# Kernel optimization log

Hardware: AMD Instinct MI355X
Metric: run time of the kernel (lower is better)

The kernel has to match this reference:

```python
import jax, jax.numpy as jnp
import numpy as np

ANG = 5  # angRes; n = ANG*ANG
EPS = 1e-12  # torch F.normalize eps

def _l2norm(x, axis):
    n = jnp.sqrt(jnp.sum(x * x, axis=axis, keepdims=True))
    return x / jnp.maximum(n, EPS)

def setup_inputs() -> dict:
    key = jax.random.key(0)
    kq, kk, kv = jax.random.split(key, 3)
    shape = (16, 16, 25, 16, 128)  # b c n h w
    return {
        "token_q": jax.random.normal(kq, shape, dtype=jnp.float32),
        "token_k": jax.random.normal(kk, shape, dtype=jnp.float32),
        "token_v": jax.random.normal(kv, shape, dtype=jnp.float32),
    }

def reference(token_q, token_k, token_v):
    b, c, n, h, w = token_q.shape
    u = v = ANG
    buffer = token_v

    def to_q(x):  # b c (u v) h w -> b (c h) (w u v)
        return x.reshape(b, c, u, v, h, w).transpose(0, 1, 4, 5, 2, 3).reshape(b, c * h, w * u * v)

    def to_k(x):  # b c (u v) h w -> b (w u v) (c h)
        return x.reshape(b, c, u, v, h, w).transpose(0, 5, 2, 3, 1, 4).reshape(b, w * u * v, c * h)

    unfold_q = _l2norm(to_q(token_q), axis=-1)      # [b, ch, wuv]
    unfold_k = _l2norm(to_k(token_k), axis=-2)      # [b, wuv, ch]
    unfold_v = to_q(token_v)                        # [b, ch, wuv]

    att = jnp.einsum('bts,bsr->btr', unfold_q, unfold_k)  # [b, ch, ch]
    size = c * h
    causal = jnp.tril(jnp.ones((size, size), dtype=bool))
    att = jnp.where(causal, att, jnp.float32(-1e15))
    att = jax.nn.softmax(att, axis=-1)

    out = jnp.einsum('btr,brs->bts', att, unfold_v)  # [b, ch, wuv]
    # b (c h) (w u v) -> b c (u v) h w
    out = out.reshape(b, c, h, w, u, v).transpose(0, 1, 4, 5, 2, 3).reshape(b, c, n, h, w)
    return out + buffer
```

## Files before the change

kernel.cpp:

```cpp
#include <hip/hip_runtime.h>
#include <math.h>

#define SB 819200
#define SC 51200
#define SN 2048
#define CH 256
#define NW 3200
#define NPARTS 10
#define PARTLEN 320
#define BK 32
#define NCH 10
#define SPART 1048576
#define G1BLOCKS 480

typedef __bf16 bf16x8 __attribute__((ext_vector_type(8)));
typedef __bf16 bf16x4 __attribute__((ext_vector_type(4)));
typedef __bf16 bf16x2 __attribute__((ext_vector_type(2)));
typedef float  f32x4  __attribute__((ext_vector_type(4)));

__device__ __forceinline__ bf16x8 cvt8(float4 a, float4 b) {
    bf16x8 r;
    r[0] = (__bf16)a.x; r[1] = (__bf16)a.y; r[2] = (__bf16)a.z; r[3] = (__bf16)a.w;
    r[4] = (__bf16)b.x; r[5] = (__bf16)b.y; r[6] = (__bf16)b.z; r[7] = (__bf16)b.w;
    return r;
}

__device__ __forceinline__ float dot4(float4 a) {
    return a.x * a.x + a.y * a.y + a.z * a.z + a.w * a.w;
}

__global__ __launch_bounds__(256, 2) void gemm1_kernel(const float* __restrict__ q,
                                                       const float* __restrict__ k,
                                                       float* __restrict__ Sp,
                                                       float* __restrict__ nq2p,
                                                       float* __restrict__ nk2p) {
    __shared__ alignas(16) float lds[16384];

    const int tid = threadIdx.x;
    const int lane = tid & 63;
    const int wave = tid >> 6;
    const int l15 = lane & 15;
    const int quad = lane >> 4;

    const int bx = blockIdx.x;
    const int tile = bx % 3;
    const int part = (bx / 3) % NPARTS;
    const int b = bx / (3 * NPARTS);
    const int tm = (tile + 1) >> 1;
    const int tn = tile >> 1;

    const int wm = wave >> 1;
    const int wn = wave & 1;

    const bool doQ = (tile != 2);
    const bool doK = (tile != 1);

    const int g8 = lane & 7;
    const int rl = lane >> 3;

    const float* qp[4];
    const float* kp[4];
#pragma unroll
    for (int i = 0; i < 4; i++) {
        const int row = wave * 32 + i * 8 + rl;
        const int ta = tm * 128 + row;
        const int rb = tn * 128 + row;
        qp[i] = q + (size_t)b * SB + (size_t)(ta >> 4) * SC + (size_t)(ta & 15) * 128 + g8 * 4;
        kp[i] = k + (size_t)b * SB + (size_t)(rb >> 4) * SC + (size_t)(rb & 15) * 128 + g8 * 4;
    }

    f32x4 acc[4][4] = {};
    bool live[4][4];
#pragma unroll
    for (int mi = 0; mi < 4; mi++)
#pragma unroll
        for (int ni = 0; ni < 4; ni++)
            live[mi][ni] = (tn * 128 + wn * 64 + ni * 16) <= (tm * 128 + wm * 64 + mi * 16);

    float sqA[4] = {0.f, 0.f, 0.f, 0.f};
    float sqB[4] = {0.f, 0.f, 0.f, 0.f};

    auto stage = [&](int ch, int p) {
        const int kg = part * PARTLEN + ch * BK;
        const size_t koff = (size_t)(kg >> 7) * SN + (kg & 127);
#pragma unroll
        for (int i = 0; i < 4; i++)
            __builtin_amdgcn_global_load_lds(
                (const __attribute__((address_space(1))) void*)(qp[i] + koff),
                (__attribute__((address_space(3))) void*)(&lds[p * 8192 + (wave * 4 + i) * 256]),
                16, 0, 0);
#pragma unroll
        for (int i = 0; i < 4; i++)
            __builtin_amdgcn_global_load_lds(
                (const __attribute__((address_space(1))) void*)(kp[i] + koff),
                (__attribute__((address_space(3))) void*)(&lds[p * 8192 + 4096 + (wave * 4 + i) * 256]),
                16, 0, 0);
    };

    stage(0, 0);

    for (int ch = 0; ch < NCH; ch++) {
        const int p = ch & 1;
        if (ch + 1 < NCH) {
            stage(ch + 1, 1 - p);
            asm volatile("s_waitcnt vmcnt(8)" ::: "memory");
        } else {
            asm volatile("s_waitcnt vmcnt(0)" ::: "memory");
        }
        __builtin_amdgcn_s_barrier();
        __builtin_amdgcn_sched_barrier(0);

        const float* A = &lds[p * 8192];
        const float* B = &lds[p * 8192 + 4096];
        bf16x8 af[4], bfr[4];
#pragma unroll
        for (int mi = 0; mi < 4; mi++) {
            const float4 lo = *(const float4*)&A[(wm * 64 + mi * 16 + l15) * 32 + quad * 8];
            const float4 hi = *(const float4*)&A[(wm * 64 + mi * 16 + l15) * 32 + quad * 8 + 4];
            af[mi] = cvt8(lo, hi);
            if (wn == 0) sqA[mi] += dot4(lo) + dot4(hi);
        }
#pragma unroll
        for (int ni = 0; ni < 4; ni++) {
            const float4 lo = *(const float4*)&B[(wn * 64 + ni * 16 + l15) * 32 + quad * 8];
            const float4 hi = *(const float4*)&B[(wn * 64 + ni * 16 + l15) * 32 + quad * 8 + 4];
            bfr[ni] = cvt8(lo, hi);
            if (wm == 0) sqB[ni] += dot4(lo) + dot4(hi);
        }
#pragma unroll
        for (int mi = 0; mi < 4; mi++)
#pragma unroll
            for (int ni = 0; ni < 4; ni++)
                if (live[mi][ni])
                    acc[mi][ni] = __builtin_amdgcn_mfma_f32_16x16x32_bf16(
                        af[mi], bfr[ni], acc[mi][ni], 0, 0, 0);

        __builtin_amdgcn_sched_barrier(0);
        __builtin_amdgcn_s_barrier();
        __builtin_amdgcn_sched_barrier(0);
    }

    float* o = Sp + (size_t)part * SPART + (size_t)b * 65536;
#pragma unroll
    for (int mi = 0; mi < 4; mi++)
#pragma unroll
        for (int ni = 0; ni < 4; ni++) {
            if (!live[mi][ni]) continue;
            const int r = tn * 128 + wn * 64 + ni * 16 + l15;
#pragma unroll
            for (int j = 0; j < 4; j++) {
                const int t = tm * 128 + wm * 64 + mi * 16 + quad * 4 + j;
                o[(size_t)t * 256 + r] = acc[mi][ni][j];
            }
        }

    if (wn == 0 && doQ) {
#pragma unroll
        for (int mi = 0; mi < 4; mi++) {
            float s = sqA[mi];
            s += __shfl_xor(s, 16, 64);
            s += __shfl_xor(s, 32, 64);
            if (lane < 16)
                nq2p[part * 4096 + b * 256 + tm * 128 + wm * 64 + mi * 16 + lane] = s;
        }
    }
    if (wm == 0 && doK) {
#pragma unroll
        for (int ni = 0; ni < 4; ni++) {
            float s = sqB[ni];
            s += __shfl_xor(s, 16, 64);
            s += __shfl_xor(s, 32, 64);
            if (lane < 16)
                nk2p[part * 4096 + b * 256 + tn * 128 + wn * 64 + ni * 16 + lane] = s;
        }
    }
}

__global__ __launch_bounds__(256) void softmax_kernel(const float* __restrict__ Sp,
                                                      const float* __restrict__ nq2p,
                                                      const float* __restrict__ nk2p,
                                                      __bf16* __restrict__ P) {
    const int wave = threadIdx.x >> 6;
    const int lane = threadIdx.x & 63;
    const int t = blockIdx.x * 4 + wave;
    const int b = blockIdx.y;
    const size_t rowbase = ((size_t)b * 256 + t) * 256;
    const int r0 = lane * 4;

    float4 s4 = {0.f, 0.f, 0.f, 0.f};
#pragma unroll
    for (int p = 0; p < NPARTS; p++) {
        const float4 x = *(const float4*)(Sp + (size_t)p * SPART + rowbase + r0);
        s4.x += x.x; s4.y += x.y; s4.z += x.z; s4.w += x.w;
    }
    float sq = 0.f;
#pragma unroll
    for (int p = 0; p < NPARTS; p++) sq += nq2p[p * 4096 + b * 256 + t];
    float4 sk = {0.f, 0.f, 0.f, 0.f};
#pragma unroll
    for (int p = 0; p < NPARTS; p++) {
        const float4 x = *(const float4*)(nk2p + p * 4096 + b * 256 + r0);
        sk.x += x.x; sk.y += x.y; sk.z += x.z; sk.w += x.w;
    }
    const float qn = 1.0f / fmaxf(sqrtf(sq), 1e-12f);
    float4 kn;
    kn.x = 1.0f / fmaxf(sqrtf(sk.x), 1e-12f);
    kn.y = 1.0f / fmaxf(sqrtf(sk.y), 1e-12f);
    kn.z = 1.0f / fmaxf(sqrtf(sk.z), 1e-12f);
    kn.w = 1.0f / fmaxf(sqrtf(sk.w), 1e-12f);

    float val[4] = {s4.x * qn * kn.x, s4.y * qn * kn.y,
                    s4.z * qn * kn.z, s4.w * qn * kn.w};
    float m = -1e30f;
#pragma unroll
    for (int j = 0; j < 4; j++) {
        if (r0 + j > t) val[j] = -1e30f;
        m = fmaxf(m, val[j]);
    }
#pragma unroll
    for (int off = 32; off; off >>= 1) m = fmaxf(m, __shfl_xor(m, off, 64));

    float e[4], sum = 0.f;
#pragma unroll
    for (int j = 0; j < 4; j++) {
        e[j] = (r0 + j <= t) ? expf(val[j] - m) : 0.f;
        sum += e[j];
    }
#pragma unroll
    for (int off = 32; off; off >>= 1) sum += __shfl_xor(sum, off, 64);

    const float inv = 1.0f / sum;
    bf16x4 o;
    o[0] = (__bf16)(e[0] * inv);
    o[1] = (__bf16)(e[1] * inv);
    o[2] = (__bf16)(e[2] * inv);
    o[3] = (__bf16)(e[3] * inv);
    *(bf16x4*)(P + rowbase + r0) = o;
}

__global__ __launch_bounds__(256, 4) void gemm2_kernel(const __bf16* __restrict__ P,
                                                       const float* __restrict__ v,
                                                       float* __restrict__ out) {
    __shared__ alignas(16) char smem[9216];
    __bf16* Vs = (__bf16*)smem;
    float* Es = (float*)smem;

    const int tid = threadIdx.x;
    const int b = blockIdx.z;
    const int tt = blockIdx.y;
    const int nw = blockIdx.x;
    const int n = nw >> 1;
    const int whalf = nw & 1;

    const int lane = tid & 63;
    const int wave = tid >> 6;
    const int wm = wave >> 1;
    const int wn = wave & 1;
    const int l15 = lane & 15;
    const int quad = lane >> 4;

    const int vu = tid & 7;
    const int rp = tid >> 3;
    const float* vbase = v + (size_t)b * SB + (size_t)n * SN + whalf * 64;

    const __bf16* Pbase = P + ((size_t)b * 256 + tt * 128 + wm * 64 + l15) * 256 + quad * 8;

    f32x4 acc[4][2] = {};

    for (int kc = 0; kc < 4; kc++) {
        bf16x8 af[4][2];
#pragma unroll
        for (int mi = 0; mi < 4; mi++)
#pragma unroll
            for (int ks = 0; ks < 2; ks++)
                af[mi][ks] = *(const bf16x8*)(Pbase + (size_t)mi * 16 * 256 + kc * 64 + ks * 32);

        float vr0[8], vr1[8];
        {
            const int r0 = kc * 64 + 2 * rp;
            const int r1 = r0 + 1;
            const float* row0 = vbase + (size_t)(r0 >> 4) * SC + (size_t)(r0 & 15) * 128;
            const float* row1 = vbase + (size_t)(r1 >> 4) * SC + (size_t)(r1 & 15) * 128;
            *(float4*)&vr0[0] = *(const float4*)(row0 + vu * 8);
            *(float4*)&vr0[4] = *(const float4*)(row0 + vu * 8 + 4);
            *(float4*)&vr1[0] = *(const float4*)(row1 + vu * 8);
            *(float4*)&vr1[4] = *(const float4*)(row1 + vu * 8 + 4);
        }
        __syncthreads();
        {
            const int rl0 = 2 * rp;
#pragma unroll
            for (int sj = 0; sj < 8; sj++) {
                const int s = vu * 8 + sj;
                bf16x2 pr;
                pr[0] = (__bf16)vr0[sj];
                pr[1] = (__bf16)vr1[sj];
                *(bf16x2*)&Vs[s * 72 + (rl0 ^ (s & 0x38))] = pr;
            }
        }
        __syncthreads();
#pragma unroll
        for (int ks = 0; ks < 2; ks++) {
            bf16x8 bfr[2];
#pragma unroll
            for (int ni = 0; ni < 2; ni++) {
                const int s = wn * 32 + ni * 16 + l15;
                bfr[ni] = *(const bf16x8*)&Vs[s * 72 + ((ks * 32 + quad * 8) ^ (s & 0x38))];
            }
#pragma unroll
            for (int mi = 0; mi < 4; mi++)
#pragma unroll
                for (int ni = 0; ni < 2; ni++)
                    acc[mi][ni] = __builtin_amdgcn_mfma_f32_16x16x32_bf16(
                        af[mi][ks], bfr[ni], acc[mi][ni], 0, 0, 0);
        }
    }

    for (int p = 0; p < 4; p++) {
        __syncthreads();
        if (wm == (p >> 1)) {
            const int mibase = (p & 1) * 2;
#pragma unroll
            for (int mm = 0; mm < 2; mm++)
#pragma unroll
                for (int ni = 0; ni < 2; ni++) {
                    const f32x4 a = acc[mibase + mm][ni];
                    const int wcol = wn * 32 + ni * 16 + l15;
#pragma unroll
                    for (int j = 0; j < 4; j++)
                        Es[(mm * 16 + quad * 4 + j) * 68 + wcol] = a[j];
                }
        }
        __syncthreads();
#pragma unroll
        for (int it = 0; it < 2; it++) {
            const int tl = it * 16 + (tid >> 4);
            const int w4 = (tid & 15) * 4;
            const int t = tt * 128 + p * 32 + tl;
            const size_t a = (size_t)b * SB + (size_t)(t >> 4) * SC + (size_t)n * SN +
                             (size_t)(t & 15) * 128 + whalf * 64 + w4;
            float4 r4 = *(const float4*)&Es[tl * 68 + w4];
            const float4 buf = *(const float4*)(v + a);
            r4.x += buf.x; r4.y += buf.y; r4.z += buf.z; r4.w += buf.w;
            *(float4*)(out + a) = r4;
        }
    }
}

extern "C" void kernel_launch(void* const* d_in, const int* in_sizes, int n_in,
                              void* d_out, int out_size, void* d_ws, size_t ws_size,
                              hipStream_t stream) {
    const float* q = (const float*)d_in[0];
    const float* k = (const float*)d_in[1];
    const float* v = (const float*)d_in[2];
    float* out = (float*)d_out;

    float* ws = (float*)d_ws;
    float* nq2p = ws;
    float* nk2p = ws + 40960;
    __bf16* P = (__bf16*)(ws + 81920);

    float* Spart = out;

    gemm1_kernel<<<dim3(G1BLOCKS), dim3(256), 0, stream>>>(q, k, Spart, nq2p, nk2p);
    softmax_kernel<<<dim3(64, 16), dim3(256), 0, stream>>>(Spart, nq2p, nk2p, P);
    gemm2_kernel<<<dim3(50, 2, 16), dim3(256), 0, stream>>>(P, v, out);
}
```

Before: 232.2 us.

## Load GEMM1 operands directly to registers with double buffering, dropping LDS staging

Replaces the LDS double-buffer staging (global_load_lds plus barriers) in gemm1 with direct per-wave global float4 loads into two register buffer sets, software-pipelined across 10 k-steps. This removes workgroup barriers and the LDS round trip. In exchange, data shared between waves is now loaded redundantly from global/L2, and register pressure rises, which may reduce occupancy under launch_bounds(256,2).

```diff
diff --git a/kernel.cpp b/kernel.cpp
--- a/kernel.cpp
+++ b/kernel.cpp
@@ -8,8 +8,7 @@
 #define NW 3200
 #define NPARTS 10
 #define PARTLEN 320
-#define BK 32
-#define NCH 10
+#define NSTEP 10
 #define SPART 1048576
 #define G1BLOCKS 480
 
@@ -34,8 +33,6 @@
                                                        float* __restrict__ Sp,
                                                        float* __restrict__ nq2p,
                                                        float* __restrict__ nk2p) {
-    __shared__ alignas(16) float lds[16384];
-
     const int tid = threadIdx.x;
     const int lane = tid & 63;
     const int wave = tid >> 6;
@@ -55,18 +52,14 @@
     const bool doQ = (tile != 2);
     const bool doK = (tile != 1);
 
-    const int g8 = lane & 7;
-    const int rl = lane >> 3;
-
-    const float* qp[4];
-    const float* kp[4];
+    const float* qrow[4];
+    const float* krow[4];
 #pragma unroll
     for (int i = 0; i < 4; i++) {
-        const int row = wave * 32 + i * 8 + rl;
-        const int ta = tm * 128 + row;
-        const int rb = tn * 128 + row;
-        qp[i] = q + (size_t)b * SB + (size_t)(ta >> 4) * SC + (size_t)(ta & 15) * 128 + g8 * 4;
-        kp[i] = k + (size_t)b * SB + (size_t)(rb >> 4) * SC + (size_t)(rb & 15) * 128 + g8 * 4;
+        const int ta = tm * 128 + wm * 64 + i * 16 + l15;
+        const int rb = tn * 128 + wn * 64 + i * 16 + l15;
+        qrow[i] = q + (size_t)b * SB + (size_t)(ta >> 4) * SC + (size_t)(ta & 15) * 128 + quad * 8;
+        krow[i] = k + (size_t)b * SB + (size_t)(rb >> 4) * SC + (size_t)(rb & 15) * 128 + quad * 8;
     }
 
     f32x4 acc[4][4] = {};
@@ -80,52 +73,36 @@
     float sqA[4] = {0.f, 0.f, 0.f, 0.f};
     float sqB[4] = {0.f, 0.f, 0.f, 0.f};
 
-    auto stage = [&](int ch, int p) {
-        const int kg = part * PARTLEN + ch * BK;
-        const size_t koff = (size_t)(kg >> 7) * SN + (kg & 127);
-#pragma unroll
-        for (int i = 0; i < 4; i++)
-            __builtin_amdgcn_global_load_lds(
-                (const __attribute__((address_space(1))) void*)(qp[i] + koff),
-                (__attribute__((address_space(3))) void*)(&lds[p * 8192 + (wave * 4 + i) * 256]),
-                16, 0, 0);
-#pragma unroll
-        for (int i = 0; i < 4; i++)
-            __builtin_amdgcn_global_load_lds(
-                (const __attribute__((address_space(1))) void*)(kp[i] + koff),
-                (__attribute__((address_space(3))) void*)(&lds[p * 8192 + 4096 + (wave * 4 + i) * 256]),
-                16, 0, 0);
+    float4 aL0[4], aH0[4], bL0[4], bH0[4];
+    float4 aL1[4], aH1[4], bL1[4], bH1[4];
+
+    auto loadstep = [&](int j, float4* aL, float4* aH, float4* bL, float4* bH) {
+        const int kgb = part * PARTLEN + j * 32;
+        const size_t koff = (size_t)(kgb >> 7) * SN + (kgb & 127);
+#pragma unroll
+        for (int i = 0; i < 4; i++) {
+            aL[i] = *(const float4*)(qrow[i] + koff);
+            aH[i] = *(const float4*)(qrow[i] + koff + 4);
+        }
+#pragma unroll
+        for (int i = 0; i < 4; i++) {
+            bL[i] = *(const float4*)(krow[i] + koff);
+            bH[i] = *(const float4*)(krow[i] + koff + 4);
+        }
     };
 
-    stage(0, 0);
-
-    for (int ch = 0; ch < NCH; ch++) {
-        const int p = ch & 1;
-        if (ch + 1 < NCH) {
-            stage(ch + 1, 1 - p);
-            asm volatile("s_waitcnt vmcnt(8)" ::: "memory");
-        } else {
-            asm volatile("s_waitcnt vmcnt(0)" ::: "memory");
-        }
-        __builtin_amdgcn_s_barrier();
-        __builtin_amdgcn_sched_barrier(0);
-
-        const float* A = &lds[p * 8192];
-        const float* B = &lds[p * 8192 + 4096];
+    auto compute = [&](const float4* aL, const float4* aH,
+                       const float4* bL, const float4* bH) {
         bf16x8 af[4], bfr[4];
 #pragma unroll
         for (int mi = 0; mi < 4; mi++) {
-            const float4 lo = *(const float4*)&A[(wm * 64 + mi * 16 + l15) * 32 + quad * 8];
-            const float4 hi = *(const float4*)&A[(wm * 64 + mi * 16 + l15) * 32 + quad * 8 + 4];
-            af[mi] = cvt8(lo, hi);
-            if (wn == 0) sqA[mi] += dot4(lo) + dot4(hi);
+            af[mi] = cvt8(aL[mi], aH[mi]);
+            if (wn == 0) sqA[mi] += dot4(aL[mi]) + dot4(aH[mi]);
         }
 #pragma unroll
         for (int ni = 0; ni < 4; ni++) {
-            const float4 lo = *(const float4*)&B[(wn * 64 + ni * 16 + l15) * 32 + quad * 8];
-            const float4 hi = *(const float4*)&B[(wn * 64 + ni * 16 + l15) * 32 + quad * 8 + 4];
-            bfr[ni] = cvt8(lo, hi);
-            if (wm == 0) sqB[ni] += dot4(lo) + dot4(hi);
+            bfr[ni] = cvt8(bL[ni], bH[ni]);
+            if (wm == 0) sqB[ni] += dot4(bL[ni]) + dot4(bH[ni]);
         }
 #pragma unroll
         for (int mi = 0; mi < 4; mi++)
@@ -134,11 +111,21 @@
                 if (live[mi][ni])
                     acc[mi][ni] = __builtin_amdgcn_mfma_f32_16x16x32_bf16(
                         af[mi], bfr[ni], acc[mi][ni], 0, 0, 0);
-
+    };
+
+    loadstep(0, aL0, aH0, bL0, bH0);
+    for (int jj = 0; jj < 4; jj++) {
+        loadstep(2 * jj + 1, aL1, aH1, bL1, bH1);
         __builtin_amdgcn_sched_barrier(0);
-        __builtin_amdgcn_s_barrier();
+        compute(aL0, aH0, bL0, bH0);
+        loadstep(2 * jj + 2, aL0, aH0, bL0, bH0);
         __builtin_amdgcn_sched_barrier(0);
-    }
+        compute(aL1, aH1, bL1, bH1);
+    }
+    loadstep(9, aL1, aH1, bL1, bH1);
+    __builtin_amdgcn_sched_barrier(0);
+    compute(aL0, aH0, bL0, bH0);
+    compute(aL1, aH1, bL1, bH1);
 
     float* o = Sp + (size_t)part * SPART + (size_t)b * 65536;
 #pragma unroll
```

Result: faster. 224.9 us (-3.2%).
